# Kernel optimization log

Measured on AMD Instinct MI355X. Metric: run time of the kernel, lower is better.

## Reference

```python
import jax, jax.numpy as jnp
import numpy as np

EPS = 1e-5

def instance_norm(x):
    # x: [B, C, H, W]; normalize over spatial dims per (b, c), no affine
    mean = jnp.mean(x, axis=(2, 3), keepdims=True)
    var = jnp.var(x, axis=(2, 3), keepdims=True)
    return (x - mean) * jax.lax.rsqrt(var + EPS)

def conv1x1(x, w, b):
    # x: [B, Cin, H, W], w: [Cout, Cin], b: [Cout]
    return jnp.einsum('bchw,oc->bohw', x, w) + b[None, :, None, None]

def setup_inputs() -> dict:
    key = jax.random.key(0)
    k1, k2, k3 = jax.random.split(key, 3)
    B, Cin, Cout, H, W = 16, 256, 256, 128, 128
    x = jax.random.normal(k1, (B, Cin, H, W), dtype=jnp.float32)
    # PyTorch Conv2d init: U(-s, s), s = 1/sqrt(fan_in) with fan_in = Cin*1*1
    s1 = 1.0 / np.sqrt(Cin)
    w1 = jax.random.uniform(k2, (Cout, Cin), jnp.float32, -s1, s1)
    b1 = jax.random.uniform(jax.random.fold_in(k2, 1), (Cout,), jnp.float32, -s1, s1)
    s2 = 1.0 / np.sqrt(Cout)
    w2 = jax.random.uniform(k3, (Cout, Cout), jnp.float32, -s2, s2)
    b2 = jax.random.uniform(jax.random.fold_in(k3, 1), (Cout,), jnp.float32, -s2, s2)
    return {"x": x, "w1": w1, "b1": b1, "w2": w2, "b2": b2}

def reference(x, w1, b1, w2, b2):
    h = jax.nn.relu(conv1x1(instance_norm(x), w1, b1))
    out = jax.nn.relu(conv1x1(instance_norm(h), w2, b2))
    return out
```

## Files before the change

kernel.cpp:

```cpp
#include <hip/hip_runtime.h>
#include <hip/hip_bf16.h>
#include <cstdint>
#include <cstddef>

#define DEVI __device__ __forceinline__

typedef unsigned short u16;
using frag_ab = __attribute__((ext_vector_type(8))) short;
using f32x4   = __attribute__((ext_vector_type(4))) float;

constexpr int HW = 16384;
constexpr int NC = 256;

DEVI u16 bf16bits(float f) {
    union { float f; uint32_t u; } cv; cv.f = f;
    uint32_t u = cv.u;
    u += 0x7fffu + ((u >> 16) & 1u);
    return (u16)(u >> 16);
}

DEVI void gload16(const void* g, void* l) {
    __builtin_amdgcn_global_load_lds(
        (const __attribute__((address_space(1))) uint32_t*)g,
        (__attribute__((address_space(3))) uint32_t*)l, 16, 0, 0);
}

DEVI frag_ab read_frag(const u16* slab, int row, int l4) {
    const int phys = (l4 ^ row ^ (row >> 2)) & 3;
    return *(const frag_ab*)((const char*)slab + row * 64 + phys * 16);
}

__global__ __launch_bounds__(256) void transpose_stats_kernel(
    const float* __restrict__ x, u16* __restrict__ xt,
    float* __restrict__ ps, float* __restrict__ pq)
{
    constexpr int PADW = 68;
    __shared__ __align__(16) u16 tile[64 * PADW];
    const int b = blockIdx.z, c0 = blockIdx.y * 64, p0 = blockIdx.x * 64;
    const int pblk = blockIdx.x;
    const int t = threadIdx.x;
    const int lane = t & 63, w = t >> 6;
    const int pq_ = lane & 15, cq = lane >> 4;
    const int quad = w * 4 + cq;
    const float* xb = x + ((size_t)b * NC + c0) * HW + p0;

    float va[4][4];
    float aS[4], aQ[4];
    #pragma unroll
    for (int j = 0; j < 4; ++j) {
        const float4 v = *(const float4*)(xb + (size_t)(quad * 4 + j) * HW + pq_ * 4);
        va[j][0] = v.x; va[j][1] = v.y; va[j][2] = v.z; va[j][3] = v.w;
        float s1 = v.x + v.y + v.z + v.w;
        float s2 = v.x*v.x + v.y*v.y + v.z*v.z + v.w*v.w;
        #pragma unroll
        for (int d = 1; d < 16; d <<= 1) {
            s1 += __shfl_xor(s1, d, 64);
            s2 += __shfl_xor(s2, d, 64);
        }
        aS[j] = s1; aQ[j] = s2;
    }
    if (pq_ == 0) {
        const float4 vs = {aS[0], aS[1], aS[2], aS[3]};
        const float4 vq = {aQ[0], aQ[1], aQ[2], aQ[3]};
        *(float4*)&ps[((size_t)b * 256 + pblk) * NC + c0 + quad * 4] = vs;
        *(float4*)&pq[((size_t)b * 256 + pblk) * NC + c0 + quad * 4] = vq;
    }
    #pragma unroll
    for (int i = 0; i < 4; ++i) {
        alignas(8) u16 pk[4];
        #pragma unroll
        for (int j = 0; j < 4; ++j) pk[j] = bf16bits(va[j][i]);
        *(uint2*)&tile[(pq_ * 4 + i) * PADW + quad * 4] = *(const uint2*)pk;
    }
    __syncthreads();
    const int pl = t >> 2, q = t & 3;
    u16* dst = xt + ((size_t)b * HW + p0 + pl) * NC + c0;
    #pragma unroll
    for (int s = 0; s < 2; ++s) {
        const int ch8 = q + s * 4;
        const uint2 lo = *(const uint2*)&tile[pl * PADW + ch8 * 8];
        const uint2 hi = *(const uint2*)&tile[pl * PADW + ch8 * 8 + 4];
        const uint4 o4 = {lo.x, lo.y, hi.x, hi.y};
        *(uint4*)(dst + ch8 * 8) = o4;
    }
}

__global__ __launch_bounds__(512) void fold_kernel(
    const float* __restrict__ w, const float* __restrict__ bias,
    const float* __restrict__ ps, const float* __restrict__ pq,
    u16* __restrict__ we, float* __restrict__ be)
{
    const int b = blockIdx.y, oc = blockIdx.x * 64;
    __shared__ float mu[NC], rs[NC];
    __shared__ float m1[2][NC], m2[2][NC];
    __shared__ __align__(16) float wt[64 * NC];
    const int t = threadIdx.x;
    {
        const int c = t & 255, half = t >> 8;
        float s1 = 0.f, s2 = 0.f;
        const float* pp = ps + (size_t)b * 256 * NC + (size_t)half * 128 * NC + c;
        const float* qq = pq + (size_t)b * 256 * NC + (size_t)half * 128 * NC + c;
        for (int i = 0; i < 128; ++i) {
            s1 += pp[(size_t)i * NC];
            s2 += qq[(size_t)i * NC];
        }
        m1[half][c] = s1; m2[half][c] = s2;
    }
    #pragma unroll
    for (int i = 0; i < 8; ++i)
        *(float4*)&wt[i*2048 + t*4] = *(const float4*)&w[(size_t)oc*NC + i*2048 + t*4];
    __syncthreads();
    if (t < NC) {
        const float s1 = m1[0][t] + m1[1][t];
        const float s2 = m2[0][t] + m2[1][t];
        const float m = s1 * (1.0f / HW);
        mu[t] = m;
        rs[t] = rsqrtf(s2 * (1.0f / HW) - m * m + 1e-5f);
    }
    __syncthreads();
    const int o = oc + (t >> 3), q = t & 7;
    const float* wrow = &wt[(t >> 3) * NC];
    u16* werow = we + ((size_t)b * NC + o) * NC;
    float bacc = 0.f;
    for (int cc = 0; cc < 4; ++cc) {
        alignas(16) u16 pk[8];
        #pragma unroll
        for (int jj = 0; jj < 8; ++jj) {
            const int c = q*32 + cc*8 + jj;
            const float wv = wrow[c];
            bacc -= wv * mu[c] * rs[c];
            pk[jj] = bf16bits(wv * rs[c]);
        }
        *(uint4*)(werow + q*32 + cc*8) = *(const uint4*)pk;
    }
    bacc += __shfl_xor(bacc, 1, 64);
    bacc += __shfl_xor(bacc, 2, 64);
    bacc += __shfl_xor(bacc, 4, 64);
    if (q == 0) be[b*NC + o] = bias[o] + bacc;
}

template<int STAGE>
__global__ __launch_bounds__(256, 2) void gemm_kernel(
    const u16* __restrict__ pixM,
    const u16* __restrict__ wMat,
    const float* __restrict__ biasE,
    u16* __restrict__ outB,
    float* __restrict__ outF,
    float* __restrict__ hps, float* __restrict__ hpq)
{
    __shared__ __align__(16) u16 ldsP[2][16384];

    const int b = blockIdx.x >> 6;
    const int g = blockIdx.x & 63;
    const int tid = threadIdx.x;
    const int lane = tid & 63, wid = tid >> 6;
    const int l15 = lane & 15, l4 = lane >> 4;

    const u16* gW = wMat + (size_t)b * NC * NC;

    const int rin  = lane >> 2;
    const int prow = wid * 16 + rin;
    const int psl  = ((lane & 3) ^ prow ^ (prow >> 2)) & 3;

    auto stageP = [&](int i, int buf) {
        const u16* gPt = pixM + ((size_t)b * HW + (g + 64 * i) * 64) * NC;
        #pragma unroll
        for (int ks = 0; ks < 8; ++ks)
            gload16(gPt + (size_t)prow * NC + ks * 32 + psl * 8,
                    (char*)ldsP[buf] + ks * 4096 + wid * 1024);
    };

    frag_ab wf[8][4];
    {
        const u16* wb = gW + (size_t)(wid * 64 + l15) * NC + l4 * 8;
        #pragma unroll
        for (int ks = 0; ks < 8; ++ks)
            #pragma unroll
            for (int f = 0; f < 4; ++f)
                wf[ks][f] = *(const frag_ab*)(wb + (size_t)f * 16 * NC + ks * 32);
    }
    float4 vb[4]; float bm[4];
    if constexpr (STAGE == 1) {
        #pragma unroll
        for (int mi = 0; mi < 4; ++mi)
            vb[mi] = *(const float4*)&biasE[b*NC + wid*64 + 16*mi + l4*4];
    } else {
        #pragma unroll
        for (int ni = 0; ni < 4; ++ni)
            bm[ni] = biasE[b*NC + wid*64 + 16*ni + l15];
    }

    stageP(0, 0);
    for (int i = 0; i < 4; ++i) {
        if (i == 0) {
            asm volatile("s_waitcnt vmcnt(0)" ::: "memory");
        } else if constexpr (STAGE == 1) {
            asm volatile("s_waitcnt vmcnt(24)" ::: "memory");
        } else {
            asm volatile("s_waitcnt vmcnt(16)" ::: "memory");
        }
        __builtin_amdgcn_s_barrier();
        if (i < 3) stageP(i + 1, (i + 1) & 1);
        asm volatile("" ::: "memory");

        f32x4 acc[4][4];
        #pragma unroll
        for (int mi = 0; mi < 4; ++mi)
            #pragma unroll
            for (int ni = 0; ni < 4; ++ni)
                acc[mi][ni] = (f32x4){0.f, 0.f, 0.f, 0.f};

        const u16* bufb = ldsP[i & 1];
        #pragma unroll
        for (int ks = 0; ks < 8; ++ks) {
            const u16* pslab = bufb + ks * 2048;
            frag_ab pf[4];
            #pragma unroll
            for (int f = 0; f < 4; ++f)
                pf[f] = read_frag(pslab, 16 * f + l15, l4);
            #pragma unroll
            for (int ni = 0; ni < 4; ++ni)
                #pragma unroll
                for (int mi = 0; mi < 4; ++mi) {
                    if constexpr (STAGE == 1)
                        acc[mi][ni] = __builtin_amdgcn_mfma_f32_16x16x32_bf16(wf[ks][mi], pf[ni], acc[mi][ni], 0, 0, 0);
                    else
                        acc[mi][ni] = __builtin_amdgcn_mfma_f32_16x16x32_bf16(pf[mi], wf[ks][ni], acc[mi][ni], 0, 0, 0);
                }
        }

        const int pblk = g + 64 * i;
        const int p0 = pblk * 64;
        if constexpr (STAGE == 1) {
            u16* htbase = outB + ((size_t)b * HW + p0) * NC + wid * 64;
            #pragma unroll
            for (int mi = 0; mi < 4; ++mi) {
                const float bx[4] = {vb[mi].x, vb[mi].y, vb[mi].z, vb[mi].w};
                float s1r[4] = {0.f,0.f,0.f,0.f}, s2r[4] = {0.f,0.f,0.f,0.f};
                #pragma unroll
                for (int ni = 0; ni < 4; ++ni) {
                    u16* rowp = htbase + (size_t)(16*ni + l15) * NC;
                    alignas(8) u16 pk[4];
                    #pragma unroll
                    for (int r = 0; r < 4; ++r) {
                        const float v = fmaxf(acc[mi][ni][r] + bx[r], 0.f);
                        s1r[r] += v; s2r[r] += v * v;
                        pk[r] = bf16bits(v);
                    }
                    *(uint2*)&rowp[16*mi + l4*4] = *(const uint2*)pk;
                }
                #pragma unroll
                for (int r = 0; r < 4; ++r) {
                    float a1 = s1r[r], a2 = s2r[r];
                    #pragma unroll
                    for (int d = 1; d < 16; d <<= 1) {
                        a1 += __shfl_xor(a1, d, 64);
                        a2 += __shfl_xor(a2, d, 64);
                    }
                    s1r[r] = a1; s2r[r] = a2;
                }
                if (l15 == 0) {
                    const int o = wid*64 + 16*mi + l4*4;
                    const float4 w1v = {s1r[0], s1r[1], s1r[2], s1r[3]};
                    const float4 w2v = {s2r[0], s2r[1], s2r[2], s2r[3]};
                    *(float4*)&hps[((size_t)b * 256 + pblk) * NC + o] = w1v;
                    *(float4*)&hpq[((size_t)b * 256 + pblk) * NC + o] = w2v;
                }
            }
        } else {
            #pragma unroll
            for (int ni = 0; ni < 4; ++ni) {
                const int o = wid*64 + 16*ni + l15;
                float* colp = outF + ((size_t)b * NC + o) * HW + p0;
                #pragma unroll
                for (int mi = 0; mi < 4; ++mi) {
                    const float4 v = {fmaxf(acc[mi][ni][0] + bm[ni], 0.f),
                                      fmaxf(acc[mi][ni][1] + bm[ni], 0.f),
                                      fmaxf(acc[mi][ni][2] + bm[ni], 0.f),
                                      fmaxf(acc[mi][ni][3] + bm[ni], 0.f)};
                    *(float4*)&colp[16*mi + l4*4] = v;
                }
            }
        }
    }
}

extern "C" void kernel_launch(void* const* d_in, const int* in_sizes, int n_in,
                              void* d_out, int out_size, void* d_ws, size_t ws_size,
                              hipStream_t stream)
{
    (void)in_sizes; (void)n_in; (void)out_size;
    const float* x  = (const float*)d_in[0];
    const float* w1 = (const float*)d_in[1];
    const float* b1 = (const float*)d_in[2];
    const float* w2 = (const float*)d_in[3];
    const float* b2 = (const float*)d_in[4];
    float* out = (float*)d_out;

    char* od = (char*)d_out;
    u16*   xt  = (u16*)od;
    float* xps = (float*)(od + 134217728);
    float* xpq = (float*)(od + 138412032);
    float* hps = (float*)(od + 142606336);
    float* hpq = (float*)(od + 146800640);

    char* ws = (char*)d_ws;
    const size_t NEED = 138444800;
    if (ws_size < NEED) return;
    u16*   ht  = (u16*)(ws);
    u16*   w1e = (u16*)(ws + 134217728);
    u16*   w2e = (u16*)(ws + 136314880);
    float* b1e = (float*)(ws + 138412032);
    float* b2e = (float*)(ws + 138428416);

    transpose_stats_kernel<<<dim3(HW/64, NC/64, 16), 256, 0, stream>>>(x, xt, xps, xpq);
    fold_kernel<<<dim3(4, 16), 512, 0, stream>>>(w1, b1, xps, xpq, w1e, b1e);
    gemm_kernel<1><<<dim3(1024), 256, 0, stream>>>(xt, w1e, b1e, ht, nullptr, hps, hpq);
    fold_kernel<<<dim3(4, 16), 512, 0, stream>>>(w2, b2, hps, hpq, w2e, b2e);
    gemm_kernel<2><<<dim3(1024), 256, 0, stream>>>(ht, w2e, b2e, nullptr, out, nullptr, nullptr);
}
```

Baseline: 302.4 us.

## Split GEMM tiles into 32-pixel strips and output-channel halves for higher occupancy

Each GEMM block now handles 32 pixels and half of the output channels instead of 64 pixels and all channels, so the grid grows to 4096 blocks. Weight fragments held in registers and LDS per block both halve, which allows 4 blocks per CU instead of 2. Stage-1 partial statistics are now written per 32-pixel strip, so the fold kernel takes a strip count and the hpq buffer offset moves. The cost is smaller MFMA tiles per wave, more redundant weight-fragment loads across blocks, and more partial-stat traffic.

```diff
diff --git a/kernel.cpp b/kernel.cpp
--- a/kernel.cpp
+++ b/kernel.cpp
@@ -87,7 +87,7 @@
 
 __global__ __launch_bounds__(512) void fold_kernel(
     const float* __restrict__ w, const float* __restrict__ bias,
-    const float* __restrict__ ps, const float* __restrict__ pq,
+    const float* __restrict__ ps, const float* __restrict__ pq, int P,
     u16* __restrict__ we, float* __restrict__ be)
 {
     const int b = blockIdx.y, oc = blockIdx.x * 64;
@@ -97,10 +97,11 @@
     const int t = threadIdx.x;
     {
         const int c = t & 255, half = t >> 8;
+        const int hp = P >> 1;
         float s1 = 0.f, s2 = 0.f;
-        const float* pp = ps + (size_t)b * 256 * NC + (size_t)half * 128 * NC + c;
-        const float* qq = pq + (size_t)b * 256 * NC + (size_t)half * 128 * NC + c;
-        for (int i = 0; i < 128; ++i) {
+        const float* pp = ps + (size_t)b * P * NC + (size_t)half * hp * NC + c;
+        const float* qq = pq + (size_t)b * P * NC + (size_t)half * hp * NC + c;
+        for (int i = 0; i < hp; ++i) {
             s1 += pp[(size_t)i * NC];
             s2 += qq[(size_t)i * NC];
         }
@@ -140,7 +141,7 @@
 }
 
 template<int STAGE>
-__global__ __launch_bounds__(256, 2) void gemm_kernel(
+__global__ __launch_bounds__(256, 4) void gemm_kernel(
     const u16* __restrict__ pixM,
     const u16* __restrict__ wMat,
     const float* __restrict__ biasE,
@@ -148,46 +149,51 @@
     float* __restrict__ outF,
     float* __restrict__ hps, float* __restrict__ hpq)
 {
-    __shared__ __align__(16) u16 ldsP[2][16384];
-
-    const int b = blockIdx.x >> 6;
-    const int g = blockIdx.x & 63;
+    __shared__ __align__(16) u16 ldsP[2][8192];
+
+    const int bx = blockIdx.x;
+    const int b = bx >> 8;
+    const int rem = bx & 255;
+    const int ohalf = rem & 1;
+    const int g = rem >> 1;
     const int tid = threadIdx.x;
     const int lane = tid & 63, wid = tid >> 6;
     const int l15 = lane & 15, l4 = lane >> 4;
+    const int rin = lane >> 2;
 
     const u16* gW = wMat + (size_t)b * NC * NC;
-
-    const int rin  = lane >> 2;
-    const int prow = wid * 16 + rin;
-    const int psl  = ((lane & 3) ^ prow ^ (prow >> 2)) & 3;
+    const int obase = ohalf * 128 + wid * 32;
 
     auto stageP = [&](int i, int buf) {
-        const u16* gPt = pixM + ((size_t)b * HW + (g + 64 * i) * 64) * NC;
+        const u16* gPt = pixM + ((size_t)b * HW + (size_t)(g + 128 * i) * 32) * NC;
+        #pragma unroll
+        for (int q = 0; q < 4; ++q) {
+            const int j = wid * 4 + q, ks = j >> 1, c = j & 1;
+            const int row = c * 16 + rin;
+            const int sl = ((lane & 3) ^ row ^ (row >> 2)) & 3;
+            gload16(gPt + (size_t)row * NC + ks * 32 + sl * 8,
+                    (char*)ldsP[buf] + j * 1024);
+        }
+    };
+
+    frag_ab wf[8][2];
+    {
+        const u16* wb = gW + (size_t)(obase + l15) * NC + l4 * 8;
         #pragma unroll
         for (int ks = 0; ks < 8; ++ks)
-            gload16(gPt + (size_t)prow * NC + ks * 32 + psl * 8,
-                    (char*)ldsP[buf] + ks * 4096 + wid * 1024);
-    };
-
-    frag_ab wf[8][4];
-    {
-        const u16* wb = gW + (size_t)(wid * 64 + l15) * NC + l4 * 8;
-        #pragma unroll
-        for (int ks = 0; ks < 8; ++ks)
-            #pragma unroll
-            for (int f = 0; f < 4; ++f)
+            #pragma unroll
+            for (int f = 0; f < 2; ++f)
                 wf[ks][f] = *(const frag_ab*)(wb + (size_t)f * 16 * NC + ks * 32);
     }
-    float4 vb[4]; float bm[4];
+    float4 vb[2]; float bm[2];
     if constexpr (STAGE == 1) {
         #pragma unroll
-        for (int mi = 0; mi < 4; ++mi)
-            vb[mi] = *(const float4*)&biasE[b*NC + wid*64 + 16*mi + l4*4];
+        for (int mi = 0; mi < 2; ++mi)
+            vb[mi] = *(const float4*)&biasE[b*NC + obase + 16*mi + l4*4];
     } else {
         #pragma unroll
-        for (int ni = 0; ni < 4; ++ni)
-            bm[ni] = biasE[b*NC + wid*64 + 16*ni + l15];
+        for (int ni = 0; ni < 2; ++ni)
+            bm[ni] = biasE[b*NC + obase + 16*ni + l15];
     }
 
     stageP(0, 0);
@@ -195,33 +201,33 @@
         if (i == 0) {
             asm volatile("s_waitcnt vmcnt(0)" ::: "memory");
         } else if constexpr (STAGE == 1) {
-            asm volatile("s_waitcnt vmcnt(24)" ::: "memory");
+            asm volatile("s_waitcnt vmcnt(8)" ::: "memory");
         } else {
-            asm volatile("s_waitcnt vmcnt(16)" ::: "memory");
+            asm volatile("s_waitcnt vmcnt(4)" ::: "memory");
         }
         __builtin_amdgcn_s_barrier();
         if (i < 3) stageP(i + 1, (i + 1) & 1);
         asm volatile("" ::: "memory");
 
-        f32x4 acc[4][4];
-        #pragma unroll
-        for (int mi = 0; mi < 4; ++mi)
-            #pragma unroll
-            for (int ni = 0; ni < 4; ++ni)
+        f32x4 acc[2][2];
+        #pragma unroll
+        for (int mi = 0; mi < 2; ++mi)
+            #pragma unroll
+            for (int ni = 0; ni < 2; ++ni)
                 acc[mi][ni] = (f32x4){0.f, 0.f, 0.f, 0.f};
 
         const u16* bufb = ldsP[i & 1];
         #pragma unroll
         for (int ks = 0; ks < 8; ++ks) {
-            const u16* pslab = bufb + ks * 2048;
-            frag_ab pf[4];
-            #pragma unroll
-            for (int f = 0; f < 4; ++f)
+            const u16* pslab = bufb + ks * 1024;
+            frag_ab pf[2];
+            #pragma unroll
+            for (int f = 0; f < 2; ++f)
                 pf[f] = read_frag(pslab, 16 * f + l15, l4);
             #pragma unroll
-            for (int ni = 0; ni < 4; ++ni)
+            for (int ni = 0; ni < 2; ++ni)
                 #pragma unroll
-                for (int mi = 0; mi < 4; ++mi) {
+                for (int mi = 0; mi < 2; ++mi) {
                     if constexpr (STAGE == 1)
                         acc[mi][ni] = __builtin_amdgcn_mfma_f32_16x16x32_bf16(wf[ks][mi], pf[ni], acc[mi][ni], 0, 0, 0);
                     else
@@ -229,21 +235,21 @@
                 }
         }
 
-        const int pblk = g + 64 * i;
-        const int p0 = pblk * 64;
+        const int strip = g + 128 * i;
+        const int p0 = strip * 32;
         if constexpr (STAGE == 1) {
-            u16* htbase = outB + ((size_t)b * HW + p0) * NC + wid * 64;
-            #pragma unroll
-            for (int mi = 0; mi < 4; ++mi) {
-                const float bx[4] = {vb[mi].x, vb[mi].y, vb[mi].z, vb[mi].w};
+            u16* htbase = outB + ((size_t)b * HW + p0) * NC + obase;
+            #pragma unroll
+            for (int mi = 0; mi < 2; ++mi) {
+                const float bx4[4] = {vb[mi].x, vb[mi].y, vb[mi].z, vb[mi].w};
                 float s1r[4] = {0.f,0.f,0.f,0.f}, s2r[4] = {0.f,0.f,0.f,0.f};
                 #pragma unroll
-                for (int ni = 0; ni < 4; ++ni) {
+                for (int ni = 0; ni < 2; ++ni) {
                     u16* rowp = htbase + (size_t)(16*ni + l15) * NC;
                     alignas(8) u16 pk[4];
                     #pragma unroll
                     for (int r = 0; r < 4; ++r) {
-                        const float v = fmaxf(acc[mi][ni][r] + bx[r], 0.f);
+                        const float v = fmaxf(acc[mi][ni][r] + bx4[r], 0.f);
                         s1r[r] += v; s2r[r] += v * v;
                         pk[r] = bf16bits(v);
                     }
@@ -260,20 +266,20 @@
                     s1r[r] = a1; s2r[r] = a2;
                 }
                 if (l15 == 0) {
-                    const int o = wid*64 + 16*mi + l4*4;
+                    const int o = obase + 16*mi + l4*4;
                     const float4 w1v = {s1r[0], s1r[1], s1r[2], s1r[3]};
                     const float4 w2v = {s2r[0], s2r[1], s2r[2], s2r[3]};
-                    *(float4*)&hps[((size_t)b * 256 + pblk) * NC + o] = w1v;
-                    *(float4*)&hpq[((size_t)b * 256 + pblk) * NC + o] = w2v;
+                    *(float4*)&hps[((size_t)b * 512 + strip) * NC + o] = w1v;
+                    *(float4*)&hpq[((size_t)b * 512 + strip) * NC + o] = w2v;
                 }
             }
         } else {
             #pragma unroll
-            for (int ni = 0; ni < 4; ++ni) {
-                const int o = wid*64 + 16*ni + l15;
+            for (int ni = 0; ni < 2; ++ni) {
+                const int o = obase + 16*ni + l15;
                 float* colp = outF + ((size_t)b * NC + o) * HW + p0;
                 #pragma unroll
-                for (int mi = 0; mi < 4; ++mi) {
+                for (int mi = 0; mi < 2; ++mi) {
                     const float4 v = {fmaxf(acc[mi][ni][0] + bm[ni], 0.f),
                                       fmaxf(acc[mi][ni][1] + bm[ni], 0.f),
                                       fmaxf(acc[mi][ni][2] + bm[ni], 0.f),
@@ -302,7 +308,7 @@
     float* xps = (float*)(od + 134217728);
     float* xpq = (float*)(od + 138412032);
     float* hps = (float*)(od + 142606336);
-    float* hpq = (float*)(od + 146800640);
+    float* hpq = (float*)(od + 150994944);
 
     char* ws = (char*)d_ws;
     const size_t NEED = 138444800;
@@ -314,8 +320,8 @@
     float* b2e = (float*)(ws + 138428416);
 
     transpose_stats_kernel<<<dim3(HW/64, NC/64, 16), 256, 0, stream>>>(x, xt, xps, xpq);
-    fold_kernel<<<dim3(4, 16), 512, 0, stream>>>(w1, b1, xps, xpq, w1e, b1e);
-    gemm_kernel<1><<<dim3(1024), 256, 0, stream>>>(xt, w1e, b1e, ht, nullptr, hps, hpq);
-    fold_kernel<<<dim3(4, 16), 512, 0, stream>>>(w2, b2, hps, hpq, w2e, b2e);
-    gemm_kernel<2><<<dim3(1024), 256, 0, stream>>>(ht, w2e, b2e, nullptr, out, nullptr, nullptr);
-}
+    fold_kernel<<<dim3(4, 16), 512, 0, stream>>>(w1, b1, xps, xpq, 256, w1e, b1e);
+    gemm_kernel<1><<<dim3(4096), 256, 0, stream>>>(xt, w1e, b1e, ht, nullptr, hps, hpq);
+    fold_kernel<<<dim3(4, 16), 512, 0, stream>>>(w2, b2, hps, hpq, 512, w2e, b2e);
+    gemm_kernel<2><<<dim3(4096), 256, 0, stream>>>(ht, w2e, b2e, nullptr, out, nullptr, nullptr);
+}
```

Measured after the change: 509.7 us. 1.69x slower.
